# Optimization experiments

Hardware: AMD Instinct MI355X
Metric: run time of the kernel (lower is better)

Reference implementation:

```python
import jax, jax.numpy as jnp
import numpy as np

BATCH, IN_WIDTH, OUT_FEATURES, FAN_IN = 512, 4096, 4096, 128

def setup_inputs() -> dict:
    key = jax.random.key(0)
    k1, k2, k3, k4 = jax.random.split(key, 4)
    input = jax.random.normal(k1, (BATCH, IN_WIDTH), dtype=jnp.float32)
    weight = jax.random.normal(k2, (OUT_FEATURES, FAN_IN), dtype=jnp.float32)
    bias = jax.random.normal(k3, (OUT_FEATURES,), dtype=jnp.float32)
    indx_seqs = jax.random.randint(k4, (OUT_FEATURES, FAN_IN), 0, IN_WIDTH, dtype=jnp.int64)
    return {"input": input, "weight": weight, "bias": bias, "indx_seqs": indx_seqs}

def reference(input, weight, bias, indx_seqs):
    # gather: (B, out_features, fan_in)
    gathered = input[:, indx_seqs]
    # elementwise mul with weight (out_features, fan_in), reduce over fan_in
    return jnp.einsum('bof,of->bo', gathered, weight) + bias
```

## Files before the change

### kernel.cpp

```cpp
#include <hip/hip_runtime.h>
#include <hip/hip_bf16.h>

#define BATCH    512
#define IN_WIDTH 4096
#define OUT_F    4096
#define FAN_IN   128

__global__ __launch_bounds__(256) void k_transpose_in(const float* __restrict__ in,
                                                      __hip_bfloat16* __restrict__ inT) {
  __shared__ float tile[32][33];
  const int jt = blockIdx.x * 32;
  const int bt = blockIdx.y * 32;
  const int tx = threadIdx.x;
  const int ty = threadIdx.y;
#pragma unroll
  for (int r = 0; r < 32; r += 8) {
    tile[ty + r][tx] = in[(size_t)(bt + ty + r) * IN_WIDTH + (jt + tx)];
  }
  __syncthreads();
#pragma unroll
  for (int r = 0; r < 32; r += 8) {
    inT[(size_t)(jt + ty + r) * BATCH + (bt + tx)] = __float2bfloat16(tile[tx][ty + r]);
  }
}

__global__ __launch_bounds__(256) void k_gather_fma(const __hip_bfloat16* __restrict__ inT,
                                                    const float* __restrict__ weight,
                                                    const float* __restrict__ bias,
                                                    const int* __restrict__ idx,
                                                    float* __restrict__ outT) {
  const int o = blockIdx.x;
  const int t = threadIdx.x;
  const int* __restrict__ idxo = idx + (size_t)o * FAN_IN;
  const float* __restrict__ wo = weight + (size_t)o * FAN_IN;
  const uint16_t* __restrict__ inTu = reinterpret_cast<const uint16_t*>(inT);

  float acc0 = 0.f, acc1 = 0.f;
#pragma unroll 8
  for (int f = 0; f < FAN_IN; ++f) {
    const int   j = idxo[f];
    const float w = wo[f];
    const uint32_t v = *reinterpret_cast<const uint32_t*>(inTu + (size_t)j * BATCH + 2 * t);
    const float lo = __uint_as_float(v << 16);
    const float hi = __uint_as_float(v & 0xffff0000u);
    acc0 = fmaf(lo, w, acc0);
    acc1 = fmaf(hi, w, acc1);
  }
  const float bz = bias[o];
  float2 r = make_float2(acc0 + bz, acc1 + bz);
  *reinterpret_cast<float2*>(outT + (size_t)o * BATCH + 2 * t) = r;
}

__global__ __launch_bounds__(256) void k_transpose_out(const float* __restrict__ outT,
                                                       float* __restrict__ out) {
  __shared__ float tile[32][33];
  const int ot = blockIdx.x * 32;
  const int bt = blockIdx.y * 32;
  const int tx = threadIdx.x;
  const int ty = threadIdx.y;
#pragma unroll
  for (int r = 0; r < 32; r += 8) {
    tile[ty + r][tx] = outT[(size_t)(ot + ty + r) * BATCH + (bt + tx)];
  }
  __syncthreads();
#pragma unroll
  for (int r = 0; r < 32; r += 8) {
    out[(size_t)(bt + ty + r) * OUT_F + (ot + tx)] = tile[tx][ty + r];
  }
}

extern "C" void kernel_launch(void* const* d_in, const int* in_sizes, int n_in,
                              void* d_out, int out_size, void* d_ws, size_t ws_size,
                              hipStream_t stream) {
  const float* input  = (const float*)d_in[0];
  const float* weight = (const float*)d_in[1];
  const float* bias   = (const float*)d_in[2];
  const int*   idx    = (const int*)d_in[3];
  float* out = (float*)d_out;

  __hip_bfloat16* inT = (__hip_bfloat16*)d_ws;
  float* outT = (float*)((char*)d_ws + (size_t)IN_WIDTH * BATCH * sizeof(__hip_bfloat16));

  dim3 tblk(32, 8);
  k_transpose_in<<<dim3(IN_WIDTH / 32, BATCH / 32), tblk, 0, stream>>>(input, inT);
  k_gather_fma<<<dim3(OUT_F), dim3(256), 0, stream>>>(inT, weight, bias, idx, outT);
  k_transpose_out<<<dim3(OUT_F / 32, BATCH / 32), tblk, 0, stream>>>(outT, out);
}
```

Measured before the change: 43.21 us.

## Fuse transposes and gather into one cooperative kernel with LDS-resident input chunks

Replaces the three kernels with a single cooperative kernel of 256 blocks. In the first phase each block transposes a slice of the input into a batch-chunked bf16 layout and packs the index/weight pairs together. After a grid-wide sync, each block loads a 16-batch chunk of the whole input width into 128KB of LDS, and each lane pair gathers from LDS for one output feature, accumulating with packed float2 FMAs and writing output directly in row-major order. This removes the output transpose and the gather's global traffic, at the cost of a grid barrier, heavy LDS use and strided output stores.

```diff
diff --git a/kernel.cpp b/kernel.cpp
--- a/kernel.cpp
+++ b/kernel.cpp
@@ -1,71 +1,123 @@
 #include <hip/hip_runtime.h>
 #include <hip/hip_bf16.h>
+#include <hip/hip_cooperative_groups.h>
 
 #define BATCH    512
 #define IN_WIDTH 4096
 #define OUT_F    4096
 #define FAN_IN   128
+#define BCHUNK   16
+#define NBG      (BATCH / BCHUNK)
+#define OBLK     512
+#define NOG      (OUT_F / OBLK)
+#define NBLOCKS  256
+#define NTHREADS 1024
+#define LDSB     (IN_WIDTH * BCHUNK * 2)
 
-__global__ __launch_bounds__(256) void k_transpose_in(const float* __restrict__ in,
-                                                      __hip_bfloat16* __restrict__ inT) {
-  __shared__ float tile[32][33];
-  const int jt = blockIdx.x * 32;
-  const int bt = blockIdx.y * 32;
-  const int tx = threadIdx.x;
-  const int ty = threadIdx.y;
+typedef float v2f __attribute__((ext_vector_type(2)));
+
+__global__ void __launch_bounds__(NTHREADS, 1)
+k_fused(const float* __restrict__ input, const int* __restrict__ idx,
+        const float* __restrict__ weight, const float* __restrict__ bias,
+        uint16_t* __restrict__ inTg, uint2* __restrict__ pk,
+        float* __restrict__ out) {
+  extern __shared__ char lds[];
+  const int t   = threadIdx.x;
+  const int blk = blockIdx.x;
+
+  {
+    float (*tile)[513] = reinterpret_cast<float (*)[513]>(lds);
+    const int bg = blk >> 3;
+    const int jt = (blk & 7) * 512;
+    const int jl = t & 511;
+    const int bh = t >> 9;
 #pragma unroll
-  for (int r = 0; r < 32; r += 8) {
-    tile[ty + r][tx] = in[(size_t)(bt + ty + r) * IN_WIDTH + (jt + tx)];
+    for (int r = 0; r < 8; ++r) {
+      const int bl = r * 2 + bh;
+      tile[bl][jl] = input[(size_t)(bg * BCHUNK + bl) * IN_WIDTH + jt + jl];
+    }
+    __syncthreads();
+    uint32_t* dst = reinterpret_cast<uint32_t*>(inTg) +
+                    ((size_t)bg * IN_WIDTH + jt) * (BCHUNK / 2);
+#pragma unroll
+    for (int k = 0; k < 4; ++k) {
+      const int d  = t + k * 1024;
+      const int jj = d >> 3;
+      const int bb = (d & 7) * 2;
+      __hip_bfloat16 h0 = __float2bfloat16(tile[bb][jj]);
+      __hip_bfloat16 h1 = __float2bfloat16(tile[bb + 1][jj]);
+      dst[d] = (uint32_t)(*reinterpret_cast<uint16_t*>(&h0)) |
+               ((uint32_t)(*reinterpret_cast<uint16_t*>(&h1)) << 16);
+    }
   }
-  __syncthreads();
+  {
+    const int i = (blk * NTHREADS + t) * 2;
+    uint4 e;
+    e.x = (uint32_t)idx[i];
+    e.y = __float_as_uint(weight[i]);
+    e.z = (uint32_t)idx[i + 1];
+    e.w = __float_as_uint(weight[i + 1]);
+    *reinterpret_cast<uint4*>(pk + i) = e;
+  }
+
+  cooperative_groups::this_grid().sync();
+
+  {
+    const int og = blk & 7;
+    const int bg = blk >> 3;
+    uint4* inS4 = reinterpret_cast<uint4*>(lds);
+    const uint4* src =
+        reinterpret_cast<const uint4*>(inTg + (size_t)bg * IN_WIDTH * BCHUNK);
 #pragma unroll
-  for (int r = 0; r < 32; r += 8) {
-    inT[(size_t)(jt + ty + r) * BATCH + (bt + tx)] = __float2bfloat16(tile[tx][ty + r]);
-  }
-}
+    for (int i = 0; i < 8; ++i) inS4[i * 1024 + t] = src[i * 1024 + t];
+    __syncthreads();
 
-__global__ __launch_bounds__(256) void k_gather_fma(const __hip_bfloat16* __restrict__ inT,
-                                                    const float* __restrict__ weight,
-                                                    const float* __restrict__ bias,
-                                                    const int* __restrict__ idx,
-                                                    float* __restrict__ outT) {
-  const int o = blockIdx.x;
-  const int t = threadIdx.x;
-  const int* __restrict__ idxo = idx + (size_t)o * FAN_IN;
-  const float* __restrict__ wo = weight + (size_t)o * FAN_IN;
-  const uint16_t* __restrict__ inTu = reinterpret_cast<const uint16_t*>(inT);
+    const int wv = t >> 6;
+    const int l  = t & 63;
+    const int o  = og * OBLK + wv * 32 + (l >> 1);
+    const int p  = l & 1;
+    const int p16 = p * 16;
 
-  float acc0 = 0.f, acc1 = 0.f;
-#pragma unroll 8
-  for (int f = 0; f < FAN_IN; ++f) {
-    const int   j = idxo[f];
-    const float w = wo[f];
-    const uint32_t v = *reinterpret_cast<const uint32_t*>(inTu + (size_t)j * BATCH + 2 * t);
-    const float lo = __uint_as_float(v << 16);
-    const float hi = __uint_as_float(v & 0xffff0000u);
-    acc0 = fmaf(lo, w, acc0);
-    acc1 = fmaf(hi, w, acc1);
-  }
-  const float bz = bias[o];
-  float2 r = make_float2(acc0 + bz, acc1 + bz);
-  *reinterpret_cast<float2*>(outT + (size_t)o * BATCH + 2 * t) = r;
-}
+    const uint4* __restrict__ pko =
+        reinterpret_cast<const uint4*>(pk + (size_t)o * FAN_IN);
+    const float bz = bias[o];
 
-__global__ __launch_bounds__(256) void k_transpose_out(const float* __restrict__ outT,
-                                                       float* __restrict__ out) {
-  __shared__ float tile[32][33];
-  const int ot = blockIdx.x * 32;
-  const int bt = blockIdx.y * 32;
-  const int tx = threadIdx.x;
-  const int ty = threadIdx.y;
+    v2f a0 = {0.f, 0.f}, a1 = {0.f, 0.f}, a2 = {0.f, 0.f}, a3 = {0.f, 0.f};
+
+    auto step = [&](uint32_t j, uint32_t wbits) {
+      const uint4 v = *reinterpret_cast<const uint4*>(lds + j * 32 + p16);
+      const float wf = __uint_as_float(wbits);
+      v2f w2; w2[0] = wf; w2[1] = wf;
+      v2f x0, x1, x2, x3;
+      x0[0] = __uint_as_float(v.x << 16); x0[1] = __uint_as_float(v.x & 0xffff0000u);
+      x1[0] = __uint_as_float(v.y << 16); x1[1] = __uint_as_float(v.y & 0xffff0000u);
+      x2[0] = __uint_as_float(v.z << 16); x2[1] = __uint_as_float(v.z & 0xffff0000u);
+      x3[0] = __uint_as_float(v.w << 16); x3[1] = __uint_as_float(v.w & 0xffff0000u);
+      a0 += x0 * w2; a1 += x1 * w2; a2 += x2 * w2; a3 += x3 * w2;
+    };
+
+    uint4 q0 = pko[0], q1 = pko[1], q2 = pko[2], q3 = pko[3];
+#pragma unroll 1
+    for (int c = 0; c < 15; ++c) {
+      const uint4 n0 = pko[c * 4 + 4];
+      const uint4 n1 = pko[c * 4 + 5];
+      const uint4 n2 = pko[c * 4 + 6];
+      const uint4 n3 = pko[c * 4 + 7];
+      step(q0.x, q0.y); step(q0.z, q0.w);
+      step(q1.x, q1.y); step(q1.z, q1.w);
+      step(q2.x, q2.y); step(q2.z, q2.w);
+      step(q3.x, q3.y); step(q3.z, q3.w);
+      q0 = n0; q1 = n1; q2 = n2; q3 = n3;
+    }
+    step(q0.x, q0.y); step(q0.z, q0.w);
+    step(q1.x, q1.y); step(q1.z, q1.w);
+    step(q2.x, q2.y); step(q2.z, q2.w);
+    step(q3.x, q3.y); step(q3.z, q3.w);
+
+    const float r[8] = {a0[0], a0[1], a1[0], a1[1], a2[0], a2[1], a3[0], a3[1]};
+    const size_t obase = (size_t)(bg * BCHUNK + p * 8) * OUT_F + o;
 #pragma unroll
-  for (int r = 0; r < 32; r += 8) {
-    tile[ty + r][tx] = outT[(size_t)(ot + ty + r) * BATCH + (bt + tx)];
-  }
-  __syncthreads();
-#pragma unroll
-  for (int r = 0; r < 32; r += 8) {
-    out[(size_t)(bt + ty + r) * OUT_F + (ot + tx)] = tile[tx][ty + r];
+    for (int i = 0; i < 8; ++i) out[obase + (size_t)i * OUT_F] = r[i] + bz;
   }
 }
 
@@ -78,11 +130,11 @@
   const int*   idx    = (const int*)d_in[3];
   float* out = (float*)d_out;
 
-  __hip_bfloat16* inT = (__hip_bfloat16*)d_ws;
-  float* outT = (float*)((char*)d_ws + (size_t)IN_WIDTH * BATCH * sizeof(__hip_bfloat16));
+  uint16_t* inTg = (uint16_t*)d_ws;
+  uint2*    pk   = (uint2*)((char*)d_ws + 4u * 1024 * 1024);
 
-  dim3 tblk(32, 8);
-  k_transpose_in<<<dim3(IN_WIDTH / 32, BATCH / 32), tblk, 0, stream>>>(input, inT);
-  k_gather_fma<<<dim3(OUT_F), dim3(256), 0, stream>>>(inT, weight, bias, idx, outT);
-  k_transpose_out<<<dim3(OUT_F / 32, BATCH / 32), tblk, 0, stream>>>(outT, out);
+  void* args[] = {(void*)&input, (void*)&idx, (void*)&weight, (void*)&bias,
+                  (void*)&inTg, (void*)&pk, (void*)&out};
+  hipLaunchCooperativeKernel((void*)k_fused, dim3(NBLOCKS), dim3(NTHREADS),
+                             args, (unsigned int)LDSB, stream);
 }
```

New measurement: 80.79 us. 87.0% more time.
